# Performance work log

Measured on AMD Instinct MI355X. Metric: run time of the kernel, lower is better.

Reference implementation:

```python
import jax, jax.numpy as jnp
import numpy as np
from jax.scipy.linalg import expm

D_MODEL, D_STATE, BATCH, SEQ_LEN = 1024, 256, 8, 2048


def setup_inputs() -> dict:
    key = jax.random.key(0)
    k0, k1, k2, k3 = jax.random.split(key, 4)
    x = jax.random.normal(k0, (BATCH, SEQ_LEN, D_MODEL), dtype=jnp.float32)
    A = jax.random.normal(k1, (D_STATE, D_STATE), dtype=jnp.float32) * 0.01
    B = jax.random.normal(k2, (D_MODEL, D_STATE), dtype=jnp.float32) * 0.01
    C = jax.random.normal(k3, (D_STATE, D_MODEL), dtype=jnp.float32) * 0.01
    D = jnp.ones((D_MODEL,), dtype=jnp.float32)
    h0 = jnp.zeros((BATCH, D_STATE), dtype=jnp.float32)
    return {"x": x, "A": A, "B": B, "C": C, "D": D, "h0": h0}


def reference(x, A, B, C, D, h0):
    # Discretized transition: matrix exponential of A * dt (dt = 0.1)
    A_d = expm(A * 0.1)  # (n, n)
    # Input projection for all timesteps at once: u_t = x_t @ B
    u = jnp.einsum('bsd,dn->bsn', x, B)  # (b, s, n)

    def step(h, u_t):
        # h_t = h_{t-1} @ A_d + x_t @ B  (matches torch bmm order: row-vec times matrix)
        h = h @ A_d + u_t  # (b, n)
        return h, h

    _, hs = jax.lax.scan(step, h0, jnp.swapaxes(u, 0, 1))  # hs: (s, b, n)
    hs = jnp.swapaxes(hs, 0, 1)  # (b, s, n)
    # y_t = h_t @ C + x_t * D
    y = jnp.einsum('bsn,nd->bsd', hs, C) + x * D
    return y
```

## Files before the change

### kernel.cpp

```cpp
#include <hip/hip_runtime.h>

typedef float f4v __attribute__((ext_vector_type(4)));
typedef short s8v __attribute__((ext_vector_type(8)));

__device__ __forceinline__ unsigned short f2bf(float x){
  union { float f; unsigned u; } v; v.f = x;
  unsigned r = v.u + 0x7fffu + ((v.u >> 16) & 1u);
  return (unsigned short)(r >> 16);
}
__device__ __forceinline__ float bf2f(unsigned short b){
  union { unsigned u; float f; } v; v.u = ((unsigned)b) << 16;
  return v.f;
}
__device__ __forceinline__ void split8(const float* __restrict__ p, s8v& h, s8v& l){
  float4 v0 = *reinterpret_cast<const float4*>(p);
  float4 v1 = *reinterpret_cast<const float4*>(p + 4);
  float a[8] = {v0.x, v0.y, v0.z, v0.w, v1.x, v1.y, v1.z, v1.w};
#pragma unroll
  for (int j = 0; j < 8; ++j) {
    unsigned short hi = f2bf(a[j]);
    h[j] = (short)hi;
    l[j] = (short)f2bf(a[j] - bf2f(hi));
  }
}
__device__ __forceinline__ void zero8(s8v& v){
#pragma unroll
  for (int j = 0; j < 8; ++j) v[j] = 0;
}

__global__ void k_prep(const float* __restrict__ A, const float* __restrict__ B,
                       const float* __restrict__ C,
                       float* __restrict__ Mt, float* __restrict__ Tp0,
                       unsigned short* __restrict__ Bt, unsigned short* __restrict__ Ct){
  int i = blockIdx.x * 256 + threadIdx.x;
  const int tot = 65536 + 262144 + 262144;
  for (; i < tot; i += gridDim.x * 256) {
    if (i < 65536) {
      int r = i >> 8, c = i & 255;
      float m = 0.1f * A[c * 256 + r];
      Mt[i] = m;
      Tp0[i] = m * 0.25f + (r == c ? 1.0f : 0.0f);
    } else if (i < 65536 + 262144) {
      int j = i - 65536;
      int n = j >> 10, k = j & 1023;
      Bt[j] = f2bf(B[k * 256 + n]);
    } else {
      int j = i - 65536 - 262144;
      int col = j >> 8, n = j & 255;
      Ct[j] = f2bf(C[n * 1024 + col]);
    }
  }
}

__global__ __launch_bounds__(256) void k_taylor(const float* __restrict__ Mt,
    const float* __restrict__ Bsrc, float* __restrict__ Odst,
    unsigned short* __restrict__ QSh, unsigned short* __restrict__ QSl,
    unsigned short* __restrict__ Et, float alpha, int fin){
  __shared__ unsigned short Bh[64][40], Bl[64][40];
  int tid = threadIdx.x, lane = tid & 63, w = tid >> 6;
  int wr = w >> 1, wc = w & 1, l15 = lane & 15, quad = lane >> 4, q8 = quad * 8;
  int bid = blockIdx.x;
  int m0 = (bid >> 2) * 64, n0 = (bid & 3) * 64;
  f4v acc[2][2] = {};
  for (int kt = 0; kt < 256; kt += 32) {
    __syncthreads();
    {
      int col = tid & 63, kk0 = (tid >> 6) * 8;
#pragma unroll
      for (int j = 0; j < 8; ++j) {
        float v = Bsrc[(kt + kk0 + j) * 256 + n0 + col];
        unsigned short hi = f2bf(v);
        Bh[col][kk0 + j] = hi;
        Bl[col][kk0 + j] = f2bf(v - bf2f(hi));
      }
    }
    __syncthreads();
#pragma unroll
    for (int aq = 0; aq < 2; ++aq) {
      s8v ah, al;
      split8(&Mt[(m0 + wr * 32 + aq * 16 + l15) * 256 + kt + q8], ah, al);
#pragma unroll
      for (int bq = 0; bq < 2; ++bq) {
        s8v bh = *reinterpret_cast<const s8v*>(&Bh[wc * 32 + bq * 16 + l15][q8]);
        s8v bl = *reinterpret_cast<const s8v*>(&Bl[wc * 32 + bq * 16 + l15][q8]);
        acc[aq][bq] = __builtin_amdgcn_mfma_f32_16x16x32_bf16(ah, bh, acc[aq][bq], 0, 0, 0);
        acc[aq][bq] = __builtin_amdgcn_mfma_f32_16x16x32_bf16(ah, bl, acc[aq][bq], 0, 0, 0);
        acc[aq][bq] = __builtin_amdgcn_mfma_f32_16x16x32_bf16(al, bh, acc[aq][bq], 0, 0, 0);
      }
    }
  }
#pragma unroll
  for (int aq = 0; aq < 2; ++aq)
#pragma unroll
    for (int bq = 0; bq < 2; ++bq)
#pragma unroll
      for (int r = 0; r < 4; ++r) {
        int gm = m0 + wr * 32 + aq * 16 + quad * 4 + r;
        int gn = n0 + wc * 32 + bq * 16 + l15;
        float raw = alpha * acc[aq][bq][r];
        float v = raw + (gm == gn ? 1.0f : 0.0f);
        if (!fin) {
          Odst[gm * 256 + gn] = v;
        } else {
          unsigned short hi = f2bf(v);
          QSh[gm * 256 + gn] = hi;
          QSl[gm * 256 + gn] = f2bf(v - bf2f(hi));
          Et[gm * 256 + gn] = f2bf(raw);
        }
      }
}

__global__ __launch_bounds__(256) void k_power(unsigned short* __restrict__ QSh,
    unsigned short* __restrict__ QSl, int d){
  __shared__ unsigned short Bh[64][40], Bl[64][40];
  int tid = threadIdx.x, lane = tid & 63, w = tid >> 6;
  int wr = w >> 1, wc = w & 1, l15 = lane & 15, quad = lane >> 4, q8 = quad * 8;
  int bid = blockIdx.x;
  int mt = bid >> 2, nt = bid & 3;
  int m0 = mt * 64, n0 = nt * 64;
  int bro = (d - 1) * 256;
  f4v acc[2][2] = {};
  for (int kt = 0; kt < 256; kt += 32) {
    __syncthreads();
    {
      int col = tid & 63, kk0 = (tid >> 6) * 8;
#pragma unroll
      for (int j = 0; j < 8; ++j) {
        int k = kt + kk0 + j;
        Bh[col][kk0 + j] = QSh[(bro + k) * 256 + n0 + col];
        Bl[col][kk0 + j] = QSl[(bro + k) * 256 + n0 + col];
      }
    }
    __syncthreads();
#pragma unroll
    for (int aq = 0; aq < 2; ++aq) {
      s8v ah = *reinterpret_cast<const s8v*>(&QSh[(m0 + wr * 32 + aq * 16 + l15) * 256 + kt + q8]);
      s8v al = *reinterpret_cast<const s8v*>(&QSl[(m0 + wr * 32 + aq * 16 + l15) * 256 + kt + q8]);
#pragma unroll
      for (int bq = 0; bq < 2; ++bq) {
        s8v bh = *reinterpret_cast<const s8v*>(&Bh[wc * 32 + bq * 16 + l15][q8]);
        s8v bl = *reinterpret_cast<const s8v*>(&Bl[wc * 32 + bq * 16 + l15][q8]);
        acc[aq][bq] = __builtin_amdgcn_mfma_f32_16x16x32_bf16(ah, bh, acc[aq][bq], 0, 0, 0);
        acc[aq][bq] = __builtin_amdgcn_mfma_f32_16x16x32_bf16(ah, bl, acc[aq][bq], 0, 0, 0);
        acc[aq][bq] = __builtin_amdgcn_mfma_f32_16x16x32_bf16(al, bh, acc[aq][bq], 0, 0, 0);
      }
    }
  }
#pragma unroll
  for (int aq = 0; aq < 2; ++aq)
#pragma unroll
    for (int bq = 0; bq < 2; ++bq)
#pragma unroll
      for (int r = 0; r < 4; ++r) {
        int gm = m0 + wr * 32 + aq * 16 + quad * 4 + r;
        int gn = n0 + wc * 32 + bq * 16 + l15;
        float v = acc[aq][bq][r];
        unsigned short hi = f2bf(v);
        QSh[(d * 256 + gm) * 256 + gn] = hi;
        QSl[(d * 256 + gm) * 256 + gn] = f2bf(v - bf2f(hi));
      }
}

__global__ __launch_bounds__(256) void k_gemm_u(const float* __restrict__ x,
                                                const unsigned short* __restrict__ Bt,
                                                unsigned short* __restrict__ u){
  int tid = threadIdx.x;
  int m0 = blockIdx.x * 32;
  int w = tid >> 6, lane = tid & 63;
  int wn = w;
  int l15 = lane & 15, quad = lane >> 4, q8 = quad * 8;
  f4v acc[4][2] = {};
  const unsigned short* bbase = Bt + (wn * 64 + l15) * 1024;
  const float* xbase = x + (size_t)(m0 + l15) * 1024;
  for (int kt = 0; kt < 1024; kt += 32) {
    s8v a[4], b[2];
#pragma unroll
    for (int nq = 0; nq < 4; ++nq)
      a[nq] = *reinterpret_cast<const s8v*>(bbase + nq * 16 * 1024 + kt + q8);
#pragma unroll
    for (int mq = 0; mq < 2; ++mq) {
      const float* p = xbase + mq * 16 * 1024 + kt + q8;
      float4 v0 = *reinterpret_cast<const float4*>(p);
      float4 v1 = *reinterpret_cast<const float4*>(p + 4);
      s8v t;
      t[0] = (short)f2bf(v0.x); t[1] = (short)f2bf(v0.y);
      t[2] = (short)f2bf(v0.z); t[3] = (short)f2bf(v0.w);
      t[4] = (short)f2bf(v1.x); t[5] = (short)f2bf(v1.y);
      t[6] = (short)f2bf(v1.z); t[7] = (short)f2bf(v1.w);
      b[mq] = t;
    }
#pragma unroll
    for (int nq = 0; nq < 4; ++nq)
#pragma unroll
      for (int mq = 0; mq < 2; ++mq)
        acc[nq][mq] = __builtin_amdgcn_mfma_f32_16x16x32_bf16(a[nq], b[mq], acc[nq][mq], 0, 0, 0);
  }
#pragma unroll
  for (int nq = 0; nq < 4; ++nq) {
    int nb = wn * 64 + nq * 16 + quad * 4;
#pragma unroll
    for (int mq = 0; mq < 2; ++mq) {
      int m = m0 + mq * 16 + l15;
      ushort4 hv;
      hv.x = f2bf(acc[nq][mq][0]); hv.y = f2bf(acc[nq][mq][1]);
      hv.z = f2bf(acc[nq][mq][2]); hv.w = f2bf(acc[nq][mq][3]);
      *reinterpret_cast<ushort4*>(&u[m * 256 + nb]) = hv;
    }
  }
}

__global__ __launch_bounds__(256, 1) void k_phase1(const unsigned short* __restrict__ u,
                                                   const unsigned short* __restrict__ Et,
                                                   unsigned short* __restrict__ hs,
                                                   float* __restrict__ g0,
                                                   const float* __restrict__ h0){
  __shared__ unsigned short hbuf[2][16][264];
  int tid = threadIdx.x, w = tid >> 6, lane = tid & 63;
  int l15 = lane & 15, quad = lane >> 4;
  int U0 = blockIdx.x * 16;
  s8v e[4][8];
#pragma unroll
  for (int ct = 0; ct < 4; ++ct) {
    int col = w * 64 + ct * 16 + l15;
#pragma unroll
    for (int kt = 0; kt < 8; ++kt)
      e[ct][kt] = *reinterpret_cast<const s8v*>(&Et[col * 256 + kt * 32 + quad * 8]);
  }
  int rowbase[4];
#pragma unroll
  for (int r = 0; r < 4; ++r) {
    int g = U0 + quad * 4 + r;
    rowbase[r] = ((g >> 7) * 2048 + (g & 127) * 16) * 256;
  }
  for (int i = tid; i < 16 * 264; i += 256) hbuf[0][0][i] = 0;
  if (blockIdx.x == 0)
    for (int i = tid; i < 2048; i += 256) g0[i] = h0[i];
  f4v acc[4] = {};
  float uv[4][4];
#pragma unroll
  for (int r = 0; r < 4; ++r)
#pragma unroll
    for (int ct = 0; ct < 4; ++ct)
      uv[r][ct] = bf2f(u[rowbase[r] + w * 64 + ct * 16 + l15]);
  __syncthreads();
  int cur = 0;
  for (int t = 0; t < 16; ++t) {
    s8v af[8];
#pragma unroll
    for (int kt = 0; kt < 8; ++kt)
      af[kt] = *reinterpret_cast<const s8v*>(&hbuf[cur][l15][kt * 32 + quad * 8]);
    float uvn[4][4];
    if (t < 15)
#pragma unroll
      for (int r = 0; r < 4; ++r)
#pragma unroll
        for (int ct = 0; ct < 4; ++ct)
          uvn[r][ct] = bf2f(u[rowbase[r] + (t + 1) * 256 + w * 64 + ct * 16 + l15]);
#pragma unroll
    for (int kt = 0; kt < 8; ++kt)
#pragma unroll
      for (int ct = 0; ct < 4; ++ct)
        acc[ct] = __builtin_amdgcn_mfma_f32_16x16x32_bf16(af[kt], e[ct][kt], acc[ct], 0, 0, 0);
    int nxt = cur ^ 1;
#pragma unroll
    for (int ct = 0; ct < 4; ++ct)
#pragma unroll
      for (int r = 0; r < 4; ++r) {
        acc[ct][r] += uv[r][ct];
        hbuf[nxt][quad * 4 + r][w * 64 + ct * 16 + l15] = f2bf(acc[ct][r]);
      }
    __syncthreads();
    int ul = w * 4 + quad, seg = l15;
    uint4 d0 = *reinterpret_cast<const uint4*>(&hbuf[nxt][ul][seg * 16]);
    uint4 d1 = *reinterpret_cast<const uint4*>(&hbuf[nxt][ul][seg * 16 + 8]);
    int g = U0 + ul;
    int hrow = ((g >> 7) * 2048 + (g & 127) * 16 + t) * 256;
    *reinterpret_cast<uint4*>(&hs[hrow + seg * 16]) = d0;
    *reinterpret_cast<uint4*>(&hs[hrow + seg * 16 + 8]) = d1;
    if (t < 15)
#pragma unroll
      for (int r = 0; r < 4; ++r)
#pragma unroll
        for (int ct = 0; ct < 4; ++ct)
          uv[r][ct] = uvn[r][ct];
    cur = nxt;
  }
#pragma unroll
  for (int ct = 0; ct < 4; ++ct)
#pragma unroll
    for (int r = 0; r < 4; ++r) {
      int g = U0 + quad * 4 + r;
      int k = g & 127, b = g >> 7;
      if (k < 127)
        g0[((k + 1) * 8 + b) * 256 + w * 64 + ct * 16 + l15] = acc[ct][r];
    }
}

__global__ __launch_bounds__(256) void k_scanround(const float* __restrict__ gi,
    float* __restrict__ go,
    const unsigned short* __restrict__ cSh, const unsigned short* __restrict__ cSl,
    unsigned short* __restrict__ dh, unsigned short* __restrict__ dl,
    int rs, int dosq){
  __shared__ unsigned short Bh[64][40], Bl[64][40];
  int tid = threadIdx.x, lane = tid & 63, w = tid >> 6;
  int l15 = lane & 15, quad = lane >> 4, q8 = quad * 8;
  int bid = blockIdx.x;
  if (bid < 256) {
    int mt = bid >> 3, nt = bid & 7;
    int mbase = mt * 32 + (w >> 1) * 16;
    int nbase = nt * 32 + (w & 1) * 16;
    f4v acc;
#pragma unroll
    for (int r = 0; r < 4; ++r)
      acc[r] = gi[(mbase + quad * 4 + r) * 256 + nbase + l15];
    int ar = mbase + l15 - rs;
    const float* arow = gi + ar * 256;
    const unsigned short* bh_row = cSh + (nbase + l15) * 256;
    const unsigned short* bl_row = cSl + (nbase + l15) * 256;
    for (int kt = 0; kt < 256; kt += 32) {
      s8v ah, al;
      if (ar >= 0) split8(arow + kt + q8, ah, al);
      else { zero8(ah); zero8(al); }
      s8v bh = *reinterpret_cast<const s8v*>(bh_row + kt + q8);
      s8v bl = *reinterpret_cast<const s8v*>(bl_row + kt + q8);
      acc = __builtin_amdgcn_mfma_f32_16x16x32_bf16(ah, bh, acc, 0, 0, 0);
      acc = __builtin_amdgcn_mfma_f32_16x16x32_bf16(ah, bl, acc, 0, 0, 0);
      acc = __builtin_amdgcn_mfma_f32_16x16x32_bf16(al, bh, acc, 0, 0, 0);
    }
#pragma unroll
    for (int r = 0; r < 4; ++r)
      go[(mbase + quad * 4 + r) * 256 + nbase + l15] = acc[r];
  } else if (dosq) {
    int wr = w >> 1, wc = w & 1;
    int t = bid - 256;
    int m0 = (t >> 2) * 64, n0 = (t & 3) * 64;
    f4v acc[2][2] = {};
    for (int kt = 0; kt < 256; kt += 32) {
      __syncthreads();
      {
        int col = tid & 63, kk0 = (tid >> 6) * 8;
#pragma unroll
        for (int j = 0; j < 8; ++j) {
          int k = kt + kk0 + j;
          Bh[col][kk0 + j] = cSh[k * 256 + n0 + col];
          Bl[col][kk0 + j] = cSl[k * 256 + n0 + col];
        }
      }
      __syncthreads();
#pragma unroll
      for (int aq = 0; aq < 2; ++aq) {
        s8v ah = *reinterpret_cast<const s8v*>(&cSh[(m0 + wr * 32 + aq * 16 + l15) * 256 + kt + q8]);
        s8v al = *reinterpret_cast<const s8v*>(&cSl[(m0 + wr * 32 + aq * 16 + l15) * 256 + kt + q8]);
#pragma unroll
        for (int bq = 0; bq < 2; ++bq) {
          s8v bh = *reinterpret_cast<const s8v*>(&Bh[wc * 32 + bq * 16 + l15][q8]);
          s8v bl = *reinterpret_cast<const s8v*>(&Bl[wc * 32 + bq * 16 + l15][q8]);
          acc[aq][bq] = __builtin_amdgcn_mfma_f32_16x16x32_bf16(ah, bh, acc[aq][bq], 0, 0, 0);
          acc[aq][bq] = __builtin_amdgcn_mfma_f32_16x16x32_bf16(ah, bl, acc[aq][bq], 0, 0, 0);
          acc[aq][bq] = __builtin_amdgcn_mfma_f32_16x16x32_bf16(al, bh, acc[aq][bq], 0, 0, 0);
        }
      }
    }
#pragma unroll
    for (int aq = 0; aq < 2; ++aq)
#pragma unroll
      for (int bq = 0; bq < 2; ++bq)
#pragma unroll
        for (int r = 0; r < 4; ++r) {
          int gm = m0 + wr * 32 + aq * 16 + quad * 4 + r;
          int gn = n0 + wc * 32 + bq * 16 + l15;
          float v = acc[aq][bq][r];
          unsigned short hi = f2bf(v);
          dh[gm * 256 + gn] = hi;
          dl[gm * 256 + gn] = f2bf(v - bf2f(hi));
        }
  }
}

__global__ __launch_bounds__(256) void k_carryexp(const float* __restrict__ g,
    const unsigned short* __restrict__ QSh, const unsigned short* __restrict__ QSl,
    unsigned short* __restrict__ hs){
  int tid = threadIdx.x, lane = tid & 63, w = tid >> 6;
  int wm = w & 1, wn = w >> 1, l15 = lane & 15, quad = lane >> 4, q8 = quad * 8;
  int t = blockIdx.x;
  int mt = t >> 6, nt = t & 63;
  int m0 = mt * 64, n0 = nt * 64;
  f4v acc[2][2] = {};
  for (int kt = 0; kt < 256; kt += 32) {
    s8v bh[2], bl[2];
#pragma unroll
    for (int mq = 0; mq < 2; ++mq)
      split8(&g[(m0 + wm * 32 + mq * 16 + l15) * 256 + kt + q8], bh[mq], bl[mq]);
#pragma unroll
    for (int nq = 0; nq < 2; ++nq) {
      int pc = n0 + wn * 32 + nq * 16 + l15;
      s8v ah = *reinterpret_cast<const s8v*>(&QSh[pc * 256 + kt + q8]);
      s8v al = *reinterpret_cast<const s8v*>(&QSl[pc * 256 + kt + q8]);
#pragma unroll
      for (int mq = 0; mq < 2; ++mq) {
        acc[nq][mq] = __builtin_amdgcn_mfma_f32_16x16x32_bf16(ah, bh[mq], acc[nq][mq], 0, 0, 0);
        acc[nq][mq] = __builtin_amdgcn_mfma_f32_16x16x32_bf16(ah, bl[mq], acc[nq][mq], 0, 0, 0);
        acc[nq][mq] = __builtin_amdgcn_mfma_f32_16x16x32_bf16(al, bh[mq], acc[nq][mq], 0, 0, 0);
      }
    }
  }
#pragma unroll
  for (int nq = 0; nq < 2; ++nq) {
    int gn = n0 + wn * 32 + nq * 16 + quad * 4;
    int t0 = gn >> 8, nn = gn & 255;
#pragma unroll
    for (int mq = 0; mq < 2; ++mq) {
      int gm = m0 + wm * 32 + mq * 16 + l15;
      int k = gm >> 3, b = gm & 7;
      int idx = (b * 2048 + k * 16 + t0) * 256 + nn;
      ushort4 hv = *reinterpret_cast<const ushort4*>(&hs[idx]);
      ushort4 ov;
      ov.x = f2bf(bf2f(hv.x) + acc[nq][mq][0]);
      ov.y = f2bf(bf2f(hv.y) + acc[nq][mq][1]);
      ov.z = f2bf(bf2f(hv.z) + acc[nq][mq][2]);
      ov.w = f2bf(bf2f(hv.w) + acc[nq][mq][3]);
      *reinterpret_cast<ushort4*>(&hs[idx]) = ov;
    }
  }
}

__global__ __launch_bounds__(256) void k_gemm_y(const unsigned short* __restrict__ hs,
                                                const unsigned short* __restrict__ Ct,
                                                const float* __restrict__ x,
                                                const float* __restrict__ D,
                                                float* __restrict__ y){
  int tid = threadIdx.x;
  int m0 = blockIdx.x * 128, n0 = blockIdx.y * 128;
  int w = tid >> 6, lane = tid & 63;
  int wm = w & 1, wn = w >> 1;
  int l15 = lane & 15, quad = lane >> 4, q8 = quad * 8;
  f4v acc[4][4] = {};
  const unsigned short* cbase = Ct + (n0 + wn * 64 + l15) * 256;
  const unsigned short* hbase = hs + (size_t)(m0 + wm * 64 + l15) * 256;
  for (int kt = 0; kt < 256; kt += 32) {
    s8v a[4], b[4];
#pragma unroll
    for (int nq = 0; nq < 4; ++nq)
      a[nq] = *reinterpret_cast<const s8v*>(cbase + nq * 16 * 256 + kt + q8);
#pragma unroll
    for (int mq = 0; mq < 4; ++mq)
      b[mq] = *reinterpret_cast<const s8v*>(hbase + mq * 16 * 256 + kt + q8);
#pragma unroll
    for (int nq = 0; nq < 4; ++nq)
#pragma unroll
      for (int mq = 0; mq < 4; ++mq)
        acc[nq][mq] = __builtin_amdgcn_mfma_f32_16x16x32_bf16(a[nq], b[mq], acc[nq][mq], 0, 0, 0);
  }
#pragma unroll
  for (int nq = 0; nq < 4; ++nq) {
    int nb = n0 + wn * 64 + nq * 16 + quad * 4;
    float4 dv = *reinterpret_cast<const float4*>(&D[nb]);
#pragma unroll
    for (int mq = 0; mq < 4; ++mq) {
      int m = m0 + wm * 64 + mq * 16 + l15;
      float4 xv = *reinterpret_cast<const float4*>(&x[(size_t)m * 1024 + nb]);
      float4 ov;
      ov.x = acc[nq][mq][0] + xv.x * dv.x;
      ov.y = acc[nq][mq][1] + xv.y * dv.y;
      ov.z = acc[nq][mq][2] + xv.z * dv.z;
      ov.w = acc[nq][mq][3] + xv.w * dv.w;
      *reinterpret_cast<float4*>(&y[(size_t)m * 1024 + nb]) = ov;
    }
  }
}

extern "C" void kernel_launch(void* const* d_in, const int* in_sizes, int n_in,
                              void* d_out, int out_size, void* d_ws, size_t ws_size,
                              hipStream_t stream) {
  (void)in_sizes; (void)n_in; (void)out_size; (void)ws_size;
  const float* x  = (const float*)d_in[0];
  const float* A  = (const float*)d_in[1];
  const float* B  = (const float*)d_in[2];
  const float* C  = (const float*)d_in[3];
  const float* D  = (const float*)d_in[4];
  const float* h0 = (const float*)d_in[5];
  float* y = (float*)d_out;

  char* ws = (char*)d_ws;
  size_t off = 0;
  auto alloc = [&](size_t bytes) { void* p = ws + off; off += (bytes + 255) & ~(size_t)255; return p; };
  float* Mt  = (float*)alloc(262144);
  float* Tp0 = (float*)alloc(262144);
  float* Tp1 = (float*)alloc(262144);
  unsigned short* QSh = (unsigned short*)alloc(2097152);
  unsigned short* QSl = (unsigned short*)alloc(2097152);
  unsigned short* Et  = (unsigned short*)alloc(131072);
  unsigned short* Sh0 = (unsigned short*)alloc(131072);
  unsigned short* Sl0 = (unsigned short*)alloc(131072);
  unsigned short* Sh1 = (unsigned short*)alloc(131072);
  unsigned short* Sl1 = (unsigned short*)alloc(131072);
  float* g0 = (float*)alloc(1048576);
  float* g1 = (float*)alloc(1048576);
  unsigned short* Bt = (unsigned short*)alloc(524288);
  unsigned short* Ct = (unsigned short*)alloc(524288);
  unsigned short* u  = (unsigned short*)alloc(8388608);
  unsigned short* hs = (unsigned short*)alloc(8388608);

  k_prep<<<2304, 256, 0, stream>>>(A, B, C, Mt, Tp0, Bt, Ct);

  k_taylor<<<16, 256, 0, stream>>>(Mt, Tp0, Tp1, QSh, QSl, Et, 1.0f / 3.0f, 0);
  k_taylor<<<16, 256, 0, stream>>>(Mt, Tp1, Tp0, QSh, QSl, Et, 0.5f, 0);
  k_taylor<<<16, 256, 0, stream>>>(Mt, Tp0, Tp1, QSh, QSl, Et, 1.0f, 1);

  for (int d = 1; d <= 8; d <<= 1)
    k_power<<<d * 16, 256, 0, stream>>>(QSh, QSl, d);

  k_gemm_u<<<512, 256, 0, stream>>>(x, Bt, u);
  k_phase1<<<64, 256, 0, stream>>>(u, Et, hs, g0, h0);

  {
    const unsigned short* cSh = QSh + 15 * 65536;
    const unsigned short* cSl = QSl + 15 * 65536;
    float* gi = g0;
    float* go = g1;
    for (int rd = 0; rd < 7; ++rd) {
      int rs = 8 << rd;
      int dosq = (rd < 6) ? 1 : 0;
      unsigned short* dh = (rd & 1) ? Sh1 : Sh0;
      unsigned short* dl = (rd & 1) ? Sl1 : Sl0;
      k_scanround<<<dosq ? 272 : 256, 256, 0, stream>>>(gi, go, cSh, cSl, dh, dl, rs, dosq);
      if (dosq) {
        cSh = dh; cSl = dl;
        float* tg = gi; gi = go; go = tg;
      }
    }
  }

  k_carryexp<<<1024, 256, 0, stream>>>(g1, QSh, QSl, hs);
  k_gemm_y<<<dim3(128, 8), 256, 0, stream>>>(hs, Ct, x, D, y);
}
```

Measured before the change: 431.0 us.

## Stage u-projection GEMM tiles through double-buffered LDS with register prefetch

The input-projection GEMM kernel now loads the x tile and the B^T tile cooperatively into a double-buffered shared-memory buffer, with each block-wide load happening once. The next k-slice is prefetched into registers while the MFMAs for the current slice run. Previously each wave read its operands straight from global memory, reading x redundantly across waves and converting it to bf16 repeatedly. This aims to cut global traffic and hide load latency, at the cost of extra LDS, a barrier on every iteration and possible bank conflicts.

After: 419.0 us. 2.8% less time.

```diff
diff --git a/kernel.cpp b/kernel.cpp
--- a/kernel.cpp
+++ b/kernel.cpp
@@ -164,40 +164,65 @@
 __global__ __launch_bounds__(256) void k_gemm_u(const float* __restrict__ x,
                                                 const unsigned short* __restrict__ Bt,
                                                 unsigned short* __restrict__ u){
+  __shared__ unsigned short lds[2][256 * 40 + 32 * 40];
   int tid = threadIdx.x;
   int m0 = blockIdx.x * 32;
   int w = tid >> 6, lane = tid & 63;
-  int wn = w;
   int l15 = lane & 15, quad = lane >> 4, q8 = quad * 8;
+  int xrow = tid >> 3, xcol = (tid & 7) * 4;
+  const float* xsrc = x + (size_t)(m0 + xrow) * 1024 + xcol;
+  const unsigned short* bsrc = Bt + (size_t)tid * 1024;
   f4v acc[4][2] = {};
-  const unsigned short* bbase = Bt + (wn * 64 + l15) * 1024;
-  const float* xbase = x + (size_t)(m0 + l15) * 1024;
-  for (int kt = 0; kt < 1024; kt += 32) {
+  float4 xr;
+  uint4 br[4];
+  xr = *reinterpret_cast<const float4*>(xsrc);
+#pragma unroll
+  for (int j = 0; j < 4; ++j)
+    br[j] = *reinterpret_cast<const uint4*>(bsrc + j * 8);
+  {
+    unsigned short* buf = lds[0];
+    ushort4 hv;
+    hv.x = f2bf(xr.x); hv.y = f2bf(xr.y); hv.z = f2bf(xr.z); hv.w = f2bf(xr.w);
+    *reinterpret_cast<ushort4*>(&buf[10240 + xrow * 40 + xcol]) = hv;
+#pragma unroll
+    for (int j = 0; j < 4; ++j)
+      *reinterpret_cast<uint4*>(&buf[tid * 40 + j * 8]) = br[j];
+  }
+  __syncthreads();
+  for (int t = 0; t < 32; ++t) {
+    unsigned short* buf  = lds[t & 1];
+    unsigned short* nbuf = lds[(t & 1) ^ 1];
+    if (t < 31) {
+      xr = *reinterpret_cast<const float4*>(xsrc + (t + 1) * 32);
+#pragma unroll
+      for (int j = 0; j < 4; ++j)
+        br[j] = *reinterpret_cast<const uint4*>(bsrc + (t + 1) * 32 + j * 8);
+    }
     s8v a[4], b[2];
 #pragma unroll
     for (int nq = 0; nq < 4; ++nq)
-      a[nq] = *reinterpret_cast<const s8v*>(bbase + nq * 16 * 1024 + kt + q8);
-#pragma unroll
-    for (int mq = 0; mq < 2; ++mq) {
-      const float* p = xbase + mq * 16 * 1024 + kt + q8;
-      float4 v0 = *reinterpret_cast<const float4*>(p);
-      float4 v1 = *reinterpret_cast<const float4*>(p + 4);
-      s8v t;
-      t[0] = (short)f2bf(v0.x); t[1] = (short)f2bf(v0.y);
-      t[2] = (short)f2bf(v0.z); t[3] = (short)f2bf(v0.w);
-      t[4] = (short)f2bf(v1.x); t[5] = (short)f2bf(v1.y);
-      t[6] = (short)f2bf(v1.z); t[7] = (short)f2bf(v1.w);
-      b[mq] = t;
-    }
+      a[nq] = *reinterpret_cast<const s8v*>(&buf[(w * 64 + nq * 16 + l15) * 40 + q8]);
+#pragma unroll
+    for (int mq = 0; mq < 2; ++mq)
+      b[mq] = *reinterpret_cast<const s8v*>(&buf[10240 + (mq * 16 + l15) * 40 + q8]);
 #pragma unroll
     for (int nq = 0; nq < 4; ++nq)
 #pragma unroll
       for (int mq = 0; mq < 2; ++mq)
         acc[nq][mq] = __builtin_amdgcn_mfma_f32_16x16x32_bf16(a[nq], b[mq], acc[nq][mq], 0, 0, 0);
+    if (t < 31) {
+      ushort4 hv;
+      hv.x = f2bf(xr.x); hv.y = f2bf(xr.y); hv.z = f2bf(xr.z); hv.w = f2bf(xr.w);
+      *reinterpret_cast<ushort4*>(&nbuf[10240 + xrow * 40 + xcol]) = hv;
+#pragma unroll
+      for (int j = 0; j < 4; ++j)
+        *reinterpret_cast<uint4*>(&nbuf[tid * 40 + j * 8]) = br[j];
+    }
+    __syncthreads();
   }
 #pragma unroll
   for (int nq = 0; nq < 4; ++nq) {
-    int nb = wn * 64 + nq * 16 + quad * 4;
+    int nb = w * 64 + nq * 16 + quad * 4;
 #pragma unroll
     for (int mq = 0; mq < 2; ++mq) {
       int m = m0 + mq * 16 + l15;
```
